# Performance work log

Hardware: AMD Instinct MI355X
Metric: run time of the kernel (lower is better)

The kernel has to match this reference:

```python
import jax, jax.numpy as jnp
import numpy as np

B, L, H = 64, 512, 512
LOC_SIZE = 100000
EPS = 1e-9
STDV = 1.0 / np.sqrt(H)


def _uniform(key, shape):
    return jax.random.uniform(key, shape, dtype=jnp.float32, minval=-STDV, maxval=STDV)


def setup_inputs() -> dict:
    key = jax.random.key(0)
    ks = jax.random.split(key, 16)
    return {
        "td_upper": jax.random.uniform(ks[0], (B, L), dtype=jnp.float32),
        "td_lower": jax.random.uniform(ks[1], (B, L), dtype=jnp.float32),
        "ld_upper": jax.random.uniform(ks[2], (B, L), dtype=jnp.float32),
        "ld_lower": jax.random.uniform(ks[3], (B, L), dtype=jnp.float32),
        "current_loc": jax.random.randint(ks[4], (B, L), 0, LOC_SIZE, dtype=jnp.int64)
            if jax.config.jax_enable_x64 else jax.random.randint(ks[4], (B, L), 0, LOC_SIZE).astype(jnp.int32),
        "loc_len": jax.random.randint(ks[5], (B,), 0, L).astype(jnp.int32),
        "weight_ih": _uniform(ks[6], (H, H)),
        "weight_th_upper": _uniform(ks[7], (H, H)),
        "weight_th_lower": _uniform(ks[8], (H, H)),
        "weight_sh_upper": _uniform(ks[9], (H, H)),
        "weight_sh_lower": _uniform(ks[10], (H, H)),
        "h0": _uniform(ks[11], (H, 1)),
        "location_weight": _uniform(ks[12], (LOC_SIZE, H)),
    }


def reference(td_upper, td_lower, ld_upper, ld_lower, current_loc, loc_len,
              weight_ih, weight_th_upper, weight_th_lower,
              weight_sh_upper, weight_sh_lower, h0, location_weight):
    # per-step mixing coefficients [B, L]
    td_den = td_upper + td_lower + EPS
    a = td_upper / td_den
    b = td_lower / td_den
    ld_den = ld_upper + ld_lower + EPS
    c = ld_upper / ld_den
    d = ld_lower / ld_den

    loc = location_weight[current_loc]  # [B, L, H]

    # ttd_j @ loc_j = a_j * (Wtu @ loc_j) + b_j * (Wtl @ loc_j)
    vt = (a[..., None] * jnp.einsum('blh,kh->blk', loc, weight_th_upper)
          + b[..., None] * jnp.einsum('blh,kh->blk', loc, weight_th_lower))
    # sld_j @ vt_j
    term = (c[..., None] * jnp.einsum('blh,kh->blk', vt, weight_sh_upper)
            + d[..., None] * jnp.einsum('blh,kh->blk', vt, weight_sh_lower))

    mask = (jnp.arange(term.shape[1])[None, :] < loc_len[:, None])  # [B, L]
    loc_vec = jnp.sum(term * mask[..., None].astype(term.dtype), axis=1)  # [B, H]

    usr_vec = (weight_ih @ h0)[:, 0]  # [H]
    return jax.nn.softmax(loc_vec + usr_vec[None, :], axis=1)
```

## Files before the change

kernel.cpp:

```cpp
#include <hip/hip_runtime.h>
#include <math.h>

constexpr int NB = 64;
constexpr int NL = 512;
constexpr int NH = 512;
#define EPSV 1e-9f


__global__ __launch_bounds__(256) void k1_gather(
    const float* __restrict__ td_u, const float* __restrict__ td_l,
    const float* __restrict__ ld_u, const float* __restrict__ ld_l,
    const int* __restrict__ cur_loc, const int* __restrict__ loc_len,
    const float* __restrict__ locw, float* __restrict__ S)
{
    const int hc  = blockIdx.x;
    const int b   = blockIdx.y;
    const int len = loc_len[b];
    const int tid = threadIdx.x;
    const int hi  = tid & 7;
    const int ls  = tid >> 3;
    const int hbase = hc * 32 + hi * 4;

    float acc[4][4];
#pragma unroll
    for (int a = 0; a < 4; ++a)
#pragma unroll
        for (int e = 0; e < 4; ++e) acc[a][e] = 0.f;

#pragma unroll 4
    for (int l = ls; l < len; l += 32) {
        const int off = b * NL + l;
        const float tu = td_u[off], tl = td_l[off];
        const float lu = ld_u[off], ll = ld_l[off];
        const float rt = 1.f / (tu + tl + EPSV);
        const float rl = 1.f / (lu + ll + EPSV);
        const float a_ = tu * rt, b_ = tl * rt;
        const float c_ = lu * rl, d_ = ll * rl;
        const float w[4] = { c_ * a_, c_ * b_, d_ * a_, d_ * b_ };
        const int idx = cur_loc[off];
        const float4 x = *(const float4*)(locw + (size_t)idx * NH + hbase);
#pragma unroll
        for (int a = 0; a < 4; ++a) {
            acc[a][0] += w[a] * x.x;
            acc[a][1] += w[a] * x.y;
            acc[a][2] += w[a] * x.z;
            acc[a][3] += w[a] * x.w;
        }
    }

#pragma unroll
    for (int a = 0; a < 4; ++a)
#pragma unroll
        for (int e = 0; e < 4; ++e) {
            float x = acc[a][e];
            x += __shfl_down(x, 32);
            x += __shfl_down(x, 16);
            x += __shfl_down(x, 8);
            acc[a][e] = x;
        }

    __shared__ float red[4][8][17];
    const int wv   = tid >> 6;
    const int lane = tid & 63;
    if (lane < 8) {
#pragma unroll
        for (int a = 0; a < 4; ++a)
#pragma unroll
            for (int e = 0; e < 4; ++e) red[wv][hi][a * 4 + e] = acc[a][e];
    }
    __syncthreads();

    if (tid < 128) {
        const int hi2 = tid & 7;
        const int v   = tid >> 3;
        const float s = red[0][hi2][v] + red[1][hi2][v]
                      + red[2][hi2][v] + red[3][hi2][v];
        const int a = v >> 2, e = v & 3;
        S[a * (NH * NB) + (hc * 32 + hi2 * 4 + e) * NB + b] = s;
    }
}

__global__ __launch_bounds__(256) void k2_vt(
    const float* __restrict__ Wtu, const float* __restrict__ Wtl,
    const float* __restrict__ S,
    float* __restrict__ Vc, float* __restrict__ Vd)
{
    const int j   = blockIdx.x;
    const int tid = threadIdx.x;

    __shared__ float wu_s[NH];
    __shared__ float wl_s[NH];
    __shared__ float comb[4][2][NB];

    {
        const float2 va = ((const float2*)(Wtu + (size_t)j * NH))[tid];
        const float2 vb = ((const float2*)(Wtl + (size_t)j * NH))[tid];
        ((float2*)wu_s)[tid] = va;
        ((float2*)wl_s)[tid] = vb;
    }
    __syncthreads();

    const int w    = tid >> 6;
    const int lane = tid & 63;
    const float* __restrict__ Sca = S;
    const float* __restrict__ Scb = S + NH * NB;
    const float* __restrict__ Sda = S + 2 * NH * NB;
    const float* __restrict__ Sdb = S + 3 * NH * NB;

    float vc0 = 0.f, vc1 = 0.f, vd0 = 0.f, vd1 = 0.f;
    const int hbeg = w * 128;
#pragma unroll 8
    for (int h = hbeg; h < hbeg + 128; h += 2) {
        const float wuA = wu_s[h],     wlA = wl_s[h];
        const float wuB = wu_s[h + 1], wlB = wl_s[h + 1];
        const int oA = h * NB + lane;
        const int oB = oA + NB;
        vc0 += wuA * Sca[oA] + wlA * Scb[oA];
        vd0 += wuA * Sda[oA] + wlA * Sdb[oA];
        vc1 += wuB * Sca[oB] + wlB * Scb[oB];
        vd1 += wuB * Sda[oB] + wlB * Sdb[oB];
    }
    comb[w][0][lane] = vc0 + vc1;
    comb[w][1][lane] = vd0 + vd1;
    __syncthreads();

    if (tid < NB) {
        Vc[j * NB + tid] = comb[0][0][tid] + comb[1][0][tid]
                         + comb[2][0][tid] + comb[3][0][tid];
    } else if (tid < 2 * NB) {
        const int ln = tid - NB;
        Vd[j * NB + ln] = comb[0][1][ln] + comb[1][1][ln]
                        + comb[2][1][ln] + comb[3][1][ln];
    }
}

__global__ __launch_bounds__(256) void k3_logits(
    const float* __restrict__ Wsu, const float* __restrict__ Wsl,
    const float* __restrict__ Wih, const float* __restrict__ h0p,
    const float* __restrict__ Vc, const float* __restrict__ Vd,
    float* __restrict__ lg)
{
    const int j   = blockIdx.x;
    const int tid = threadIdx.x;

    __shared__ float su_s[NH];
    __shared__ float sl_s[NH];
    __shared__ float ih_s[NH];
    __shared__ float h0_s[NH];
    __shared__ float comb[4][64];
    __shared__ float comb_u[4];

    {
        const float2 va = ((const float2*)(Wsu + (size_t)j * NH))[tid];
        const float2 vb = ((const float2*)(Wsl + (size_t)j * NH))[tid];
        const float2 vi = ((const float2*)(Wih + (size_t)j * NH))[tid];
        const float2 vh = ((const float2*)h0p)[tid];
        ((float2*)su_s)[tid] = va;
        ((float2*)sl_s)[tid] = vb;
        ((float2*)ih_s)[tid] = vi;
        ((float2*)h0_s)[tid] = vh;
    }
    __syncthreads();

    const int w    = tid >> 6;
    const int lane = tid & 63;

    float s0 = 0.f, s1 = 0.f, u = 0.f;
    const int kbeg = w * 128;
#pragma unroll 8
    for (int k = kbeg; k < kbeg + 128; k += 2) {
        const float aA = su_s[k],     cA = sl_s[k];
        const float aB = su_s[k + 1], cB = sl_s[k + 1];
        const int oA = k * NB + lane;
        const int oB = oA + NB;
        s0 += aA * Vc[oA] + cA * Vd[oA];
        s1 += aB * Vc[oB] + cB * Vd[oB];
        u  += ih_s[k] * h0_s[k] + ih_s[k + 1] * h0_s[k + 1];
    }
    comb[w][lane] = s0 + s1;
    if (lane == 0) comb_u[w] = u;
    __syncthreads();

    if (tid < NB) {
        const float s = comb[0][tid] + comb[1][tid] + comb[2][tid] + comb[3][tid];
        const float usr = comb_u[0] + comb_u[1] + comb_u[2] + comb_u[3];
        lg[j * NB + tid] = s + usr;
    }
}

__global__ __launch_bounds__(512) void k4_softmax(
    const float* __restrict__ lg, float* __restrict__ out)
{
    const int b = blockIdx.x;
    const int j = threadIdx.x;
    __shared__ float sd[512];

    const float v = lg[j * NB + b];
    sd[j] = v;
    __syncthreads();
    for (int s = 256; s > 0; s >>= 1) {
        if (j < s) sd[j] = fmaxf(sd[j], sd[j + s]);
        __syncthreads();
    }
    const float m = sd[0];
    __syncthreads();
    const float e = expf(v - m);
    sd[j] = e;
    __syncthreads();
    for (int s = 256; s > 0; s >>= 1) {
        if (j < s) sd[j] += sd[j + s];
        __syncthreads();
    }
    const float denom = sd[0];
    out[b * NH + j] = e / denom;
}

extern "C" void kernel_launch(void* const* d_in, const int* in_sizes, int n_in,
                              void* d_out, int out_size, void* d_ws, size_t ws_size,
                              hipStream_t stream)
{
    const float* td_u = (const float*)d_in[0];
    const float* td_l = (const float*)d_in[1];
    const float* ld_u = (const float*)d_in[2];
    const float* ld_l = (const float*)d_in[3];
    const int*   cloc = (const int*)d_in[4];
    const int*   llen = (const int*)d_in[5];
    const float* Wih  = (const float*)d_in[6];
    const float* Wtu  = (const float*)d_in[7];
    const float* Wtl  = (const float*)d_in[8];
    const float* Wsu  = (const float*)d_in[9];
    const float* Wsl  = (const float*)d_in[10];
    const float* h0   = (const float*)d_in[11];
    const float* locw = (const float*)d_in[12];

    float* S  = (float*)d_ws;
    float* Vc = S  + 4 * NH * NB;
    float* Vd = Vc + NH * NB;
    float* lg = Vd + NH * NB;
    float* out = (float*)d_out;

    k1_gather<<<dim3(NH / 32, NB), 256, 0, stream>>>(
        td_u, td_l, ld_u, ld_l, cloc, llen, locw, S);
    k2_vt<<<NH, 256, 0, stream>>>(Wtu, Wtl, S, Vc, Vd);
    k3_logits<<<NH, 256, 0, stream>>>(Wsu, Wsl, Wih, h0, Vc, Vd, lg);
    k4_softmax<<<NB, 512, 0, stream>>>(lg, out);
}
```

Before: 311.1 us.

## Compute four output rows per block in k2/k3 to reuse S and V loads

```diff
diff --git a/kernel.cpp b/kernel.cpp
--- a/kernel.cpp
+++ b/kernel.cpp
@@ -60,9 +60,8 @@
         }
 
     __shared__ float red[4][8][17];
-    const int wv   = tid >> 6;
-    const int lane = tid & 63;
-    if (lane < 8) {
+    const int wv = tid >> 6;
+    if ((tid & 63) < 8) {
 #pragma unroll
         for (int a = 0; a < 4; ++a)
 #pragma unroll
@@ -85,18 +84,20 @@
     const float* __restrict__ S,
     float* __restrict__ Vc, float* __restrict__ Vd)
 {
-    const int j   = blockIdx.x;
+    const int j0  = blockIdx.x * 4;
     const int tid = threadIdx.x;
 
-    __shared__ float wu_s[NH];
-    __shared__ float wl_s[NH];
-    __shared__ float comb[4][2][NB];
+    __shared__ float wu_s[4][NH];
+    __shared__ float wl_s[4][NH];
+    __shared__ float comb[4][4][2][NB];
 
     {
-        const float2 va = ((const float2*)(Wtu + (size_t)j * NH))[tid];
-        const float2 vb = ((const float2*)(Wtl + (size_t)j * NH))[tid];
-        ((float2*)wu_s)[tid] = va;
-        ((float2*)wl_s)[tid] = vb;
+        const float4* su = (const float4*)(Wtu + (size_t)j0 * NH);
+        const float4* sl = (const float4*)(Wtl + (size_t)j0 * NH);
+        float4* du = (float4*)&wu_s[0][0];
+        float4* dl = (float4*)&wl_s[0][0];
+        du[tid] = su[tid];  du[tid + 256] = su[tid + 256];
+        dl[tid] = sl[tid];  dl[tid + 256] = sl[tid + 256];
     }
     __syncthreads();
 
@@ -107,30 +108,37 @@
     const float* __restrict__ Sda = S + 2 * NH * NB;
     const float* __restrict__ Sdb = S + 3 * NH * NB;
 
-    float vc0 = 0.f, vc1 = 0.f, vd0 = 0.f, vd1 = 0.f;
+    float vc[4] = {0.f, 0.f, 0.f, 0.f};
+    float vd[4] = {0.f, 0.f, 0.f, 0.f};
     const int hbeg = w * 128;
-#pragma unroll 8
-    for (int h = hbeg; h < hbeg + 128; h += 2) {
-        const float wuA = wu_s[h],     wlA = wl_s[h];
-        const float wuB = wu_s[h + 1], wlB = wl_s[h + 1];
-        const int oA = h * NB + lane;
-        const int oB = oA + NB;
-        vc0 += wuA * Sca[oA] + wlA * Scb[oA];
-        vd0 += wuA * Sda[oA] + wlA * Sdb[oA];
-        vc1 += wuB * Sca[oB] + wlB * Scb[oB];
-        vd1 += wuB * Sda[oB] + wlB * Sdb[oB];
-    }
-    comb[w][0][lane] = vc0 + vc1;
-    comb[w][1][lane] = vd0 + vd1;
-    __syncthreads();
-
-    if (tid < NB) {
-        Vc[j * NB + tid] = comb[0][0][tid] + comb[1][0][tid]
-                         + comb[2][0][tid] + comb[3][0][tid];
-    } else if (tid < 2 * NB) {
-        const int ln = tid - NB;
-        Vd[j * NB + ln] = comb[0][1][ln] + comb[1][1][ln]
-                        + comb[2][1][ln] + comb[3][1][ln];
+#pragma unroll 4
+    for (int h = hbeg; h < hbeg + 128; ++h) {
+        const int o = h * NB + lane;
+        const float sca = Sca[o], scb = Scb[o];
+        const float sda = Sda[o], sdb = Sdb[o];
+#pragma unroll
+        for (int j = 0; j < 4; ++j) {
+            const float wu = wu_s[j][h], wl = wl_s[j][h];
+            vc[j] += wu * sca + wl * scb;
+            vd[j] += wu * sda + wl * sdb;
+        }
+    }
+#pragma unroll
+    for (int j = 0; j < 4; ++j) {
+        comb[w][j][0][lane] = vc[j];
+        comb[w][j][1][lane] = vd[j];
+    }
+    __syncthreads();
+
+#pragma unroll
+    for (int t = tid; t < 512; t += 256) {
+        const int j  = t >> 7;
+        const int io = (t >> 6) & 1;
+        const int ln = t & 63;
+        const float v = comb[0][j][io][ln] + comb[1][j][io][ln]
+                      + comb[2][j][io][ln] + comb[3][j][io][ln];
+        if (io == 0) Vc[(j0 + j) * NB + ln] = v;
+        else         Vd[(j0 + j) * NB + ln] = v;
     }
 }
 
@@ -140,51 +148,62 @@
     const float* __restrict__ Vc, const float* __restrict__ Vd,
     float* __restrict__ lg)
 {
-    const int j   = blockIdx.x;
+    const int j0  = blockIdx.x * 4;
     const int tid = threadIdx.x;
 
-    __shared__ float su_s[NH];
-    __shared__ float sl_s[NH];
-    __shared__ float ih_s[NH];
+    __shared__ float su_s[4][NH];
+    __shared__ float sl_s[4][NH];
+    __shared__ float ih_s[4][NH];
     __shared__ float h0_s[NH];
-    __shared__ float comb[4][64];
-    __shared__ float comb_u[4];
+    __shared__ float comb[4][4][NB];
+    __shared__ float comb_u[4][4];
 
     {
-        const float2 va = ((const float2*)(Wsu + (size_t)j * NH))[tid];
-        const float2 vb = ((const float2*)(Wsl + (size_t)j * NH))[tid];
-        const float2 vi = ((const float2*)(Wih + (size_t)j * NH))[tid];
-        const float2 vh = ((const float2*)h0p)[tid];
-        ((float2*)su_s)[tid] = va;
-        ((float2*)sl_s)[tid] = vb;
-        ((float2*)ih_s)[tid] = vi;
-        ((float2*)h0_s)[tid] = vh;
+        const float4* su = (const float4*)(Wsu + (size_t)j0 * NH);
+        const float4* sl = (const float4*)(Wsl + (size_t)j0 * NH);
+        const float4* ih = (const float4*)(Wih + (size_t)j0 * NH);
+        float4* dsu = (float4*)&su_s[0][0];
+        float4* dsl = (float4*)&sl_s[0][0];
+        float4* dih = (float4*)&ih_s[0][0];
+        dsu[tid] = su[tid];  dsu[tid + 256] = su[tid + 256];
+        dsl[tid] = sl[tid];  dsl[tid + 256] = sl[tid + 256];
+        dih[tid] = ih[tid];  dih[tid + 256] = ih[tid + 256];
+        if (tid < 128) ((float4*)h0_s)[tid] = ((const float4*)h0p)[tid];
     }
     __syncthreads();
 
     const int w    = tid >> 6;
     const int lane = tid & 63;
 
-    float s0 = 0.f, s1 = 0.f, u = 0.f;
+    float s[4] = {0.f, 0.f, 0.f, 0.f};
+    float u[4] = {0.f, 0.f, 0.f, 0.f};
     const int kbeg = w * 128;
-#pragma unroll 8
-    for (int k = kbeg; k < kbeg + 128; k += 2) {
-        const float aA = su_s[k],     cA = sl_s[k];
-        const float aB = su_s[k + 1], cB = sl_s[k + 1];
-        const int oA = k * NB + lane;
-        const int oB = oA + NB;
-        s0 += aA * Vc[oA] + cA * Vd[oA];
-        s1 += aB * Vc[oB] + cB * Vd[oB];
-        u  += ih_s[k] * h0_s[k] + ih_s[k + 1] * h0_s[k + 1];
-    }
-    comb[w][lane] = s0 + s1;
-    if (lane == 0) comb_u[w] = u;
-    __syncthreads();
-
-    if (tid < NB) {
-        const float s = comb[0][tid] + comb[1][tid] + comb[2][tid] + comb[3][tid];
-        const float usr = comb_u[0] + comb_u[1] + comb_u[2] + comb_u[3];
-        lg[j * NB + tid] = s + usr;
+#pragma unroll 4
+    for (int k = kbeg; k < kbeg + 128; ++k) {
+        const int o = k * NB + lane;
+        const float vcv = Vc[o], vdv = Vd[o];
+        const float h0v = h0_s[k];
+#pragma unroll
+        for (int j = 0; j < 4; ++j) {
+            s[j] += su_s[j][k] * vcv + sl_s[j][k] * vdv;
+            u[j] += ih_s[j][k] * h0v;
+        }
+    }
+#pragma unroll
+    for (int j = 0; j < 4; ++j) {
+        comb[w][j][lane] = s[j];
+        if (lane == 0) comb_u[w][j] = u[j];
+    }
+    __syncthreads();
+
+    {
+        const int b  = tid >> 2;
+        const int jj = tid & 3;
+        const float sv = comb[0][jj][b] + comb[1][jj][b]
+                       + comb[2][jj][b] + comb[3][jj][b];
+        const float uv = comb_u[0][jj] + comb_u[1][jj]
+                       + comb_u[2][jj] + comb_u[3][jj];
+        lg[b * NH + j0 + jj] = sv + uv;
     }
 }
 
@@ -195,7 +214,7 @@
     const int j = threadIdx.x;
     __shared__ float sd[512];
 
-    const float v = lg[j * NB + b];
+    const float v = lg[b * NH + j];
     sd[j] = v;
     __syncthreads();
     for (int s = 256; s > 0; s >>= 1) {
@@ -241,7 +260,7 @@
 
     k1_gather<<<dim3(NH / 32, NB), 256, 0, stream>>>(
         td_u, td_l, ld_u, ld_l, cloc, llen, locw, S);
-    k2_vt<<<NH, 256, 0, stream>>>(Wtu, Wtl, S, Vc, Vd);
-    k3_logits<<<NH, 256, 0, stream>>>(Wsu, Wsl, Wih, h0, Vc, Vd, lg);
+    k2_vt<<<NH / 4, 256, 0, stream>>>(Wtu, Wtl, S, Vc, Vd);
+    k3_logits<<<NH / 4, 256, 0, stream>>>(Wsu, Wsl, Wih, h0, Vc, Vd, lg);
     k4_softmax<<<NB, 512, 0, stream>>>(lg, out);
 }
```

New measurement: 330.6 us. +6.3%, slower.
